# Kernel optimization log

Measured on AMD Instinct MI355X. Metric: run time of the kernel, lower is better.

## Reference

```python
import jax, jax.numpy as jnp
import numpy as np

N = 8192
E = 131072
IN = 512
H = 8
C = 128
HC = H * C
EPS = 1e-5
NEG_SLOPE = 0.2


def _gatv2(x, src, dst, Wl, bl, Wr, br, att, bias):
    """GATv2Conv (PyG semantics, concat=True, self-loops already in src/dst)."""
    n = x.shape[0]
    xl = (x @ Wl + bl).reshape(n, H, C)  # source transform (lin_l)
    xr = (x @ Wr + br).reshape(n, H, C)  # dest transform (lin_r)
    m = xl[src] + xr[dst]                # [E,H,C] per-edge message
    e = jnp.einsum('ehc,hc->eh', jax.nn.leaky_relu(m, NEG_SLOPE), att)  # [E,H]
    # segment softmax over destination nodes
    emax = jax.ops.segment_max(e, dst, num_segments=n)
    w = jnp.exp(e - emax[dst])
    denom = jax.ops.segment_sum(w, dst, num_segments=n)
    alpha = w / denom[dst]               # [E,H]
    out = jax.ops.segment_sum(alpha[:, :, None] * xl[src], dst, num_segments=n)
    return out.reshape(n, HC) + bias


def _bn(x, gamma, beta):
    mu = jnp.mean(x, axis=0)
    var = jnp.mean((x - mu) ** 2, axis=0)
    return (x - mu) * jax.lax.rsqrt(var + EPS) * gamma + beta


def setup_inputs() -> dict:
    key = jax.random.key(0)
    ks = jax.random.split(key, 16)
    s = 0.05
    return {
        'x': jax.random.normal(ks[0], (N, IN), jnp.float32),
        'edge_index': jax.random.randint(ks[1], (2, E), 0, N, jnp.int32),
        'W1l': jax.random.normal(ks[2], (IN, HC), jnp.float32) * s,
        'b1l': jnp.zeros((HC,), jnp.float32),
        'W1r': jax.random.normal(ks[3], (IN, HC), jnp.float32) * s,
        'b1r': jnp.zeros((HC,), jnp.float32),
        'att1': jax.random.normal(ks[4], (H, C), jnp.float32) * s,
        'bias1': jnp.zeros((HC,), jnp.float32),
        'g1': jnp.ones((HC,), jnp.float32),
        'beta1': jnp.zeros((HC,), jnp.float32),
        'W2l': jax.random.normal(ks[5], (HC, HC), jnp.float32) * s,
        'b2l': jnp.zeros((HC,), jnp.float32),
        'W2r': jax.random.normal(ks[6], (HC, HC), jnp.float32) * s,
        'b2r': jnp.zeros((HC,), jnp.float32),
        'att2': jax.random.normal(ks[7], (H, C), jnp.float32) * s,
        'bias2': jnp.zeros((HC,), jnp.float32),
        'g2': jnp.ones((HC,), jnp.float32),
        'beta2': jnp.zeros((HC,), jnp.float32),
    }


def reference(x, edge_index, W1l, b1l, W1r, b1r, att1, bias1, g1, beta1,
              W2l, b2l, W2r, b2r, att2, bias2, g2, beta2):
    n = x.shape[0]
    loops = jnp.arange(n, dtype=edge_index.dtype)
    src = jnp.concatenate([edge_index[0], loops])
    dst = jnp.concatenate([edge_index[1], loops])
    h = _gatv2(x, src, dst, W1l, b1l, W1r, b1r, att1, bias1)
    h = jax.nn.elu(_bn(h, g1, beta1))
    h = _gatv2(h, src, dst, W2l, b2l, W2r, b2r, att2, bias2)
    h = jax.nn.elu(_bn(h, g2, beta2))
    return h
```

## Files before the change

kernel.cpp:

```cpp
#include <hip/hip_runtime.h>
#include <stdint.h>

#define NN     8192
#define NEDGE  131072
#define NETOT  (NEDGE + NN)
#define K_IN   512
#define HC_    1024
#define NOUT   2048
#define BNEPS  1e-5f
#define SLOPE  0.2f

typedef __bf16 bf16x8 __attribute__((ext_vector_type(8)));
typedef float  f32x4  __attribute__((ext_vector_type(4)));
typedef float  f32x2  __attribute__((ext_vector_type(2)));

__device__ __forceinline__ float bf2f(unsigned short u) {
  union { uint32_t u; float f; } c; c.u = ((uint32_t)u) << 16; return c.f;
}
__device__ __forceinline__ unsigned short f2bf(float f) {
  union { float f; uint32_t u; } c; c.f = f;
  uint32_t r = c.u + 0x7fffu + ((c.u >> 16) & 1u);
  return (unsigned short)(r >> 16);
}
__device__ __forceinline__ f32x2 upk2(uint32_t u) {
  union { uint32_t u; float f; } a, b;
  a.u = u << 16; b.u = u & 0xffff0000u;
  f32x2 r; r.x = a.f; r.y = b.f; return r;
}

__device__ __forceinline__ void gload16(const void* g, void* l) {
  __builtin_amdgcn_global_load_lds(
      (const __attribute__((address_space(1))) uint32_t*)g,
      (__attribute__((address_space(3))) uint32_t*)l, 16, 0, 0);
}

#define SBAR() do { asm volatile("" ::: "memory"); __builtin_amdgcn_s_barrier(); asm volatile("" ::: "memory"); } while (0)

__global__ __launch_bounds__(256) void k_cvt_bf16(const float* __restrict__ in,
                                                  unsigned short* __restrict__ out, int n4) {
  int i = blockIdx.x * 256 + threadIdx.x;
  if (i >= n4) return;
  float4 v = *(const float4*)&in[(size_t)i * 4];
  ushort4 o;
  o.x = f2bf(v.x); o.y = f2bf(v.y); o.z = f2bf(v.z); o.w = f2bf(v.w);
  *(ushort4*)&out[(size_t)i * 4] = o;
}

__global__ __launch_bounds__(256) void k_transpose2_bf16(const float* __restrict__ Wa,
                                                         const float* __restrict__ Wb,
                                                         unsigned short* __restrict__ Wt,
                                                         int K, int N) {
  __shared__ float tile[32][33];
  const float* W = blockIdx.z ? Wb : Wa;
  unsigned short* dst = Wt + (size_t)blockIdx.z * N * K;
  int n0 = blockIdx.x * 32, k0 = blockIdx.y * 32;
  int tx = threadIdx.x & 31, ty = threadIdx.x >> 5;
  for (int i = ty; i < 32; i += 8)
    tile[i][tx] = W[(size_t)(k0 + i) * N + n0 + tx];
  __syncthreads();
  for (int i = ty; i < 32; i += 8)
    dst[(size_t)(n0 + i) * K + k0 + tx] = f2bf(tile[tx][i]);
}

__global__ __launch_bounds__(256) void k_hist(const int* __restrict__ ei, int* __restrict__ cnt) {
  int i = blockIdx.x * 256 + threadIdx.x;
  if (i >= NETOT) return;
  int d = (i < NEDGE) ? ei[NEDGE + i] : (i - NEDGE);
  atomicAdd(&cnt[d], 1);
}

__global__ __launch_bounds__(256) void k_scan(const int* __restrict__ cnt,
                                              int* __restrict__ rowptr,
                                              int* __restrict__ cursor) {
  __shared__ int part[256];
  int t = threadIdx.x;
  int base = t * 32;
  int s = 0;
  for (int i = 0; i < 32; ++i) s += cnt[base + i];
  part[t] = s;
  __syncthreads();
  for (int off = 1; off < 256; off <<= 1) {
    int u = (t >= off) ? part[t - off] : 0;
    __syncthreads();
    part[t] += u;
    __syncthreads();
  }
  int run = part[t] - s;
  for (int i = 0; i < 32; ++i) {
    rowptr[base + i] = run;
    cursor[base + i] = run;
    run += cnt[base + i];
  }
  if (t == 255) rowptr[NN] = run;
}

__global__ __launch_bounds__(256) void k_scatter(const int* __restrict__ ei,
                                                 int* __restrict__ cursor,
                                                 int* __restrict__ srcs) {
  int i = blockIdx.x * 256 + threadIdx.x;
  if (i >= NETOT) return;
  int s, d;
  if (i < NEDGE) { s = ei[i]; d = ei[NEDGE + i]; }
  else           { s = d = i - NEDGE; }
  int pos = atomicAdd(&cursor[d], 1);
  srcs[pos] = s;
}

__global__ __launch_bounds__(512, 2) void k_gemm256(const unsigned short* __restrict__ A,
                                                    const unsigned short* __restrict__ Bt,
                                                    const float* __restrict__ biasL,
                                                    const float* __restrict__ biasR,
                                                    unsigned short* __restrict__ C,
                                                    int K) {
  __shared__ unsigned short lA[2][256 * 64];
  __shared__ unsigned short lB[2][256 * 64];

  const int bid = blockIdx.x;
  const int xcd = bid & 7, idx = bid >> 3;
  const int m0 = (xcd * 4 + (idx & 3)) * 256;
  const int n0 = (idx >> 2) * 256;

  const int tid = threadIdx.x;
  const int l   = tid & 63;
  const int wv  = tid >> 6;
  const int wm  = wv >> 2, wn = wv & 3;
  const int l15 = l & 15, l4 = l >> 4;

  const int srow = tid >> 3;
  const int ssgk = (tid & 7) ^ (srow & 7);

  const f32x4 vzero = {0.f, 0.f, 0.f, 0.f};
  f32x4 acc[8][4];
#pragma unroll
  for (int i = 0; i < 8; ++i)
#pragma unroll
    for (int j = 0; j < 4; ++j) acc[i][j] = vzero;

  bf16x8 a2[8];
  bf16x8 bb[2][4];

  auto stageA = [&](int kt, int h) {
    const int buf = kt & 1;
    const size_t go = (size_t)(m0 + h * 128 + srow) * K + (size_t)kt * 64 + ssgk * 8;
    unsigned short* lp = &lA[buf][h * 8192 + tid * 8];
    gload16(&A[go], lp);
    gload16(&A[go + (size_t)64 * K], lp + 4096);
  };
  auto stageB = [&](int kt, int h) {
    const int buf = kt & 1;
    const size_t go = (size_t)(n0 + h * 128 + srow) * K + (size_t)kt * 64 + ssgk * 8;
    unsigned short* lp = &lB[buf][h * 8192 + tid * 8];
    gload16(&Bt[go], lp);
    gload16(&Bt[go + (size_t)64 * K], lp + 4096);
  };
  auto readA = [&](int buf, int qm) {
#pragma unroll
    for (int fm = 0; fm < 4; ++fm)
#pragma unroll
      for (int kk = 0; kk < 2; ++kk) {
        int r = wm * 128 + (qm * 4 + fm) * 16 + l15;
        int g = (kk * 4 + l4) ^ (r & 7);
        a2[fm * 2 + kk] = *(const bf16x8*)&lA[buf][r * 64 + g * 8];
      }
  };
  auto readB = [&](int buf, int qn) {
#pragma unroll
    for (int fn = 0; fn < 2; ++fn)
#pragma unroll
      for (int kk = 0; kk < 2; ++kk) {
        int r = wn * 64 + (qn * 2 + fn) * 16 + l15;
        int g = (kk * 4 + l4) ^ (r & 7);
        bb[qn][fn * 2 + kk] = *(const bf16x8*)&lB[buf][r * 64 + g * 8];
      }
  };
  auto quad = [&](int qm, int qn) {
    __builtin_amdgcn_s_setprio(1);
#pragma unroll
    for (int fm = 0; fm < 4; ++fm)
#pragma unroll
      for (int fn = 0; fn < 2; ++fn)
#pragma unroll
        for (int kk = 0; kk < 2; ++kk)
          acc[qm * 4 + fm][qn * 2 + fn] = __builtin_amdgcn_mfma_f32_16x16x32_bf16(
              a2[fm * 2 + kk], bb[qn][fn * 2 + kk], acc[qm * 4 + fm][qn * 2 + fn], 0, 0, 0);
    __builtin_amdgcn_s_setprio(0);
  };

  const int NT = K >> 6;

  stageA(0, 0); stageA(0, 1); stageB(0, 0); stageB(0, 1);
  if (NT > 1) stageA(1, 0);
  asm volatile("s_waitcnt vmcnt(2)" ::: "memory");
  SBAR();

  for (int t = 0; t < NT; ++t) {
    const int buf = t & 1;
    readA(buf, 0); readB(buf, 0);
    if (t + 1 < NT) stageA(t + 1, 1);
    SBAR();
    quad(0, 0);
    SBAR();
    readB(buf, 1);
    if (t + 1 < NT) stageB(t + 1, 0);
    SBAR();
    quad(0, 1);
    SBAR();
    readA(buf, 1);
    if (t + 1 < NT) stageB(t + 1, 1);
    SBAR();
    quad(1, 0);
    SBAR();
    if (t + 2 < NT) stageA(t + 2, 0);
    asm volatile("s_waitcnt vmcnt(2)" ::: "memory");
    SBAR();
    quad(1, 1);
    SBAR();
  }

  const float* bias = (n0 < HC_) ? biasL : (biasR - HC_);
#pragma unroll
  for (int fm = 0; fm < 8; ++fm) {
#pragma unroll
    for (int fn = 0; fn < 4; ++fn) {
      int col = n0 + wn * 64 + fn * 16 + l15;
      float bv = bias[col];
#pragma unroll
      for (int j = 0; j < 4; ++j) {
        int row = m0 + wm * 128 + fm * 16 + l4 * 4 + j;
        C[(size_t)row * NOUT + col] = f2bf(acc[fm][fn][j] + bv);
      }
    }
  }
}

template <bool OUT_BF16>
__global__ __launch_bounds__(256) void k_edge_agg(const unsigned short* __restrict__ XLR,
                                                  const float* __restrict__ att,
                                                  const float* __restrict__ bias,
                                                  const int* __restrict__ rowptr,
                                                  const int* __restrict__ srcs,
                                                  void* __restrict__ outp) {
  const int tid = threadIdx.x;
  const int d   = blockIdx.x * 4 + (tid >> 6);
  const int l   = tid & 63;
  const int c0  = l * 16;

  f32x2 attv[8], xrv[8];
  {
    const f32x2* ap = (const f32x2*)&att[c0];
#pragma unroll
    for (int q = 0; q < 8; ++q) attv[q] = ap[q];
    const uint4* rp = (const uint4*)&XLR[(size_t)d * NOUT + HC_ + c0];
    uint4 u0 = rp[0], u1 = rp[1];
    xrv[0] = upk2(u0.x); xrv[1] = upk2(u0.y); xrv[2] = upk2(u0.z); xrv[3] = upk2(u0.w);
    xrv[4] = upk2(u1.x); xrv[5] = upk2(u1.y); xrv[6] = upk2(u1.z); xrv[7] = upk2(u1.w);
  }

  f32x2 acc[8];
#pragma unroll
  for (int j = 0; j < 8; ++j) acc[j] = (f32x2){0.f, 0.f};
  float den = 0.f;

  const int beg = rowptr[d], end = rowptr[d + 1];

  uint4 A0, A1, B0, B1, C0, C1;
  {
    const uint4* rp = (const uint4*)&XLR[(size_t)srcs[beg] * NOUT + c0];
    A0 = rp[0]; A1 = rp[1];
  }
  if (beg + 1 < end) {
    const uint4* rp = (const uint4*)&XLR[(size_t)srcs[beg + 1] * NOUT + c0];
    B0 = rp[0]; B1 = rp[1];
  }
  if (beg + 2 < end) {
    const uint4* rp = (const uint4*)&XLR[(size_t)srcs[beg + 2] * NOUT + c0];
    C0 = rp[0]; C1 = rp[1];
  }
  int sD = (beg + 3 < end) ? srcs[beg + 3] : 0;
  int sE = (beg + 4 < end) ? srcs[beg + 4] : 0;

  int i = beg;

#define EDGE_STEP(X0, X1)                                                      \
  {                                                                            \
    f32x2 x[8];                                                                \
    x[0] = upk2(X0.x); x[1] = upk2(X0.y); x[2] = upk2(X0.z); x[3] = upk2(X0.w);\
    x[4] = upk2(X1.x); x[5] = upk2(X1.y); x[6] = upk2(X1.z); x[7] = upk2(X1.w);\
    if (i + 3 < end) {                                                         \
      const uint4* rp = (const uint4*)&XLR[(size_t)sD * NOUT + c0];            \
      X0 = rp[0]; X1 = rp[1];                                                  \
    }                                                                          \
    sD = sE;                                                                   \
    if (i + 5 < end) sE = srcs[i + 5];                                         \
    f32x2 ps = (f32x2){0.f, 0.f};                                              \
    _Pragma("unroll")                                                          \
    for (int j = 0; j < 8; ++j) {                                              \
      f32x2 y  = x[j] + xrv[j];                                                \
      f32x2 lr = __builtin_elementwise_max(y, y * SLOPE);                      \
      ps = lr * attv[j] + ps;                                                  \
    }                                                                          \
    float p = ps.x + ps.y;                                                     \
    p += __shfl_xor(p, 1);                                                     \
    p += __shfl_xor(p, 2);                                                     \
    p += __shfl_xor(p, 4);                                                     \
    float wgt = __expf(p);                                                     \
    den += wgt;                                                                \
    f32x2 w2 = (f32x2){wgt, wgt};                                              \
    _Pragma("unroll")                                                          \
    for (int j = 0; j < 8; ++j) acc[j] = w2 * x[j] + acc[j];                   \
    ++i;                                                                       \
  }

  while (true) {
    EDGE_STEP(A0, A1); if (i >= end) break;
    EDGE_STEP(B0, B1); if (i >= end) break;
    EDGE_STEP(C0, C1); if (i >= end) break;
  }
#undef EDGE_STEP

  float inv = 1.0f / den;
  float o[16];
#pragma unroll
  for (int j = 0; j < 8; ++j) {
    f32x2 bv = ((const f32x2*)&bias[c0])[j];
    o[j * 2]     = acc[j].x * inv + bv.x;
    o[j * 2 + 1] = acc[j].y * inv + bv.y;
  }
  if (OUT_BF16) {
    unsigned short* op = (unsigned short*)outp + (size_t)d * HC_ + c0;
    ushort4 u[4];
#pragma unroll
    for (int q = 0; q < 4; ++q) {
      u[q].x = f2bf(o[q * 4 + 0]); u[q].y = f2bf(o[q * 4 + 1]);
      u[q].z = f2bf(o[q * 4 + 2]); u[q].w = f2bf(o[q * 4 + 3]);
      *(ushort4*)&op[q * 4] = u[q];
    }
  } else {
    float* op = (float*)outp + (size_t)d * HC_ + c0;
#pragma unroll
    for (int q = 0; q < 4; ++q) {
      float4 ov = {o[q * 4 + 0], o[q * 4 + 1], o[q * 4 + 2], o[q * 4 + 3]};
      *(float4*)&op[q * 4] = ov;
    }
  }
}

template <bool IN_BF16>
__global__ __launch_bounds__(256) void k_colstats(const void* __restrict__ Xp,
                                                  float* __restrict__ stats) {
  int col = blockIdx.x * 256 + threadIdx.x;
  int r0 = blockIdx.y * 128;
  float s = 0.f, q = 0.f;
  for (int r = r0; r < r0 + 128; ++r) {
    float v = IN_BF16 ? bf2f(((const unsigned short*)Xp)[(size_t)r * HC_ + col])
                      : ((const float*)Xp)[(size_t)r * HC_ + col];
    s += v;
    q += v * v;
  }
  atomicAdd(&stats[col], s);
  atomicAdd(&stats[HC_ + col], q);
}

template <bool IN_BF16, bool OUT_BF16>
__global__ __launch_bounds__(256) void k_bn_elu(const void* __restrict__ Xp,
                                                const float* __restrict__ stats,
                                                const float* __restrict__ gamma,
                                                const float* __restrict__ beta,
                                                void* __restrict__ outp) {
  size_t idx = (size_t)blockIdx.x * 256 + threadIdx.x;
  size_t e0 = idx * 4;
  int col = (int)(e0 & (HC_ - 1));
  float xs[4];
  if (IN_BF16) {
    ushort4 u = *(const ushort4*)&((const unsigned short*)Xp)[e0];
    xs[0] = bf2f(u.x); xs[1] = bf2f(u.y); xs[2] = bf2f(u.z); xs[3] = bf2f(u.w);
  } else {
    float4 xv = *(const float4*)&((const float*)Xp)[e0];
    xs[0] = xv.x; xs[1] = xv.y; xs[2] = xv.z; xs[3] = xv.w;
  }
  float os[4];
  const float rn = 1.0f / (float)NN;
#pragma unroll
  for (int j = 0; j < 4; ++j) {
    int c = col + j;
    float mu = stats[c] * rn;
    float var = stats[HC_ + c] * rn - mu * mu;
    float v = (xs[j] - mu) * rsqrtf(var + BNEPS) * gamma[c] + beta[c];
    os[j] = v > 0.f ? v : (__expf(v) - 1.f);
  }
  if (OUT_BF16) {
    ushort4 o;
    o.x = f2bf(os[0]); o.y = f2bf(os[1]); o.z = f2bf(os[2]); o.w = f2bf(os[3]);
    *(ushort4*)&((unsigned short*)outp)[e0] = o;
  } else {
    float4 o = {os[0], os[1], os[2], os[3]};
    *(float4*)&((float*)outp)[e0] = o;
  }
}

extern "C" void kernel_launch(void* const* d_in, const int* in_sizes, int n_in,
                              void* d_out, int out_size, void* d_ws, size_t ws_size,
                              hipStream_t stream) {
  const float* x     = (const float*)d_in[0];
  const int*   ei    = (const int*)d_in[1];
  const float* W1l   = (const float*)d_in[2];
  const float* b1l   = (const float*)d_in[3];
  const float* W1r   = (const float*)d_in[4];
  const float* b1r   = (const float*)d_in[5];
  const float* att1  = (const float*)d_in[6];
  const float* bias1 = (const float*)d_in[7];
  const float* g1    = (const float*)d_in[8];
  const float* be1   = (const float*)d_in[9];
  const float* W2l   = (const float*)d_in[10];
  const float* b2l   = (const float*)d_in[11];
  const float* W2r   = (const float*)d_in[12];
  const float* b2r   = (const float*)d_in[13];
  const float* att2  = (const float*)d_in[14];
  const float* bias2 = (const float*)d_in[15];
  const float* g2    = (const float*)d_in[16];
  const float* be2   = (const float*)d_in[17];
  float* out = (float*)d_out;

  char* wsb = (char*)d_ws;
  size_t o = 0;
  auto alloc = [&](size_t b) {
    void* p = wsb + o;
    o = (o + b + 255) & ~(size_t)255;
    return p;
  };
  unsigned short* xbf  = (unsigned short*)alloc((size_t)NN * K_IN * 2);
  unsigned short* wT1  = (unsigned short*)alloc((size_t)NOUT * K_IN * 2);
  unsigned short* wT2  = (unsigned short*)alloc((size_t)NOUT * HC_ * 2);
  unsigned short* XLR  = (unsigned short*)alloc((size_t)NN * NOUT * 2);
  unsigned short* h0   = (unsigned short*)alloc((size_t)NN * HC_ * 2);
  int* cnt     = (int*)alloc((size_t)NN * 4);
  int* rowptr  = (int*)alloc((size_t)(NN + 1) * 4);
  int* cursor  = (int*)alloc((size_t)NN * 4);
  int* srcs    = (int*)alloc((size_t)NETOT * 4);
  float* stats = (float*)alloc((size_t)2 * HC_ * 4);

  hipMemsetAsync(cnt, 0, (size_t)NN * 4, stream);
  hipMemsetAsync(stats, 0, (size_t)2 * HC_ * 4, stream);

  k_cvt_bf16<<<(NN * K_IN / 4 + 255) / 256, 256, 0, stream>>>(x, xbf, NN * K_IN / 4);
  k_transpose2_bf16<<<dim3(HC_ / 32, K_IN / 32, 2), 256, 0, stream>>>(W1l, W1r, wT1, K_IN, HC_);
  k_transpose2_bf16<<<dim3(HC_ / 32, HC_ / 32, 2), 256, 0, stream>>>(W2l, W2r, wT2, HC_, HC_);

  k_hist<<<(NETOT + 255) / 256, 256, 0, stream>>>(ei, cnt);
  k_scan<<<1, 256, 0, stream>>>(cnt, rowptr, cursor);
  k_scatter<<<(NETOT + 255) / 256, 256, 0, stream>>>(ei, cursor, srcs);

  k_gemm256<<<256, 512, 0, stream>>>(xbf, wT1, b1l, b1r, XLR, K_IN);
  k_edge_agg<true><<<NN / 4, 256, 0, stream>>>(XLR, att1, bias1, rowptr, srcs, h0);
  k_colstats<true><<<dim3(HC_ / 256, NN / 128), 256, 0, stream>>>(h0, stats);
  k_bn_elu<true, true><<<NN * HC_ / 4 / 256, 256, 0, stream>>>(h0, stats, g1, be1, h0);

  k_gemm256<<<256, 512, 0, stream>>>(h0, wT2, b2l, b2r, XLR, HC_);
  k_edge_agg<true><<<NN / 4, 256, 0, stream>>>(XLR, att2, bias2, rowptr, srcs, h0);
  hipMemsetAsync(stats, 0, (size_t)2 * HC_ * 4, stream);
  k_colstats<true><<<dim3(HC_ / 256, NN / 128), 256, 0, stream>>>(h0, stats);
  k_bn_elu<true, false><<<NN * HC_ / 4 / 256, 256, 0, stream>>>(h0, stats, g2, be2, out);
}
```

Baseline: 248.6 us.

## Split each destination node across two waves in edge aggregation

New measurement: 233.3 us, median of 3. -6.2%, faster.

```diff
diff --git a/kernel.cpp b/kernel.cpp
--- a/kernel.cpp
+++ b/kernel.cpp
@@ -234,114 +234,99 @@
 }
 
 template <bool OUT_BF16>
-__global__ __launch_bounds__(256) void k_edge_agg(const unsigned short* __restrict__ XLR,
-                                                  const float* __restrict__ att,
-                                                  const float* __restrict__ bias,
-                                                  const int* __restrict__ rowptr,
-                                                  const int* __restrict__ srcs,
-                                                  void* __restrict__ outp) {
-  const int tid = threadIdx.x;
-  const int d   = blockIdx.x * 4 + (tid >> 6);
-  const int l   = tid & 63;
-  const int c0  = l * 16;
-
-  f32x2 attv[8], xrv[8];
+__global__ __launch_bounds__(256, 8) void k_edge_agg(const unsigned short* __restrict__ XLR,
+                                                     const float* __restrict__ att,
+                                                     const float* __restrict__ bias,
+                                                     const int* __restrict__ rowptr,
+                                                     const int* __restrict__ srcs,
+                                                     void* __restrict__ outp) {
+  const int tid  = threadIdx.x;
+  const int wv   = tid >> 6;
+  const int d    = blockIdx.x * 2 + (wv >> 1);
+  const int half = wv & 1;
+  const int l    = tid & 63;
+  const int c0   = half * 512 + l * 8;
+
+  f32x2 attv[4], xrv[4];
   {
     const f32x2* ap = (const f32x2*)&att[c0];
-#pragma unroll
-    for (int q = 0; q < 8; ++q) attv[q] = ap[q];
-    const uint4* rp = (const uint4*)&XLR[(size_t)d * NOUT + HC_ + c0];
-    uint4 u0 = rp[0], u1 = rp[1];
-    xrv[0] = upk2(u0.x); xrv[1] = upk2(u0.y); xrv[2] = upk2(u0.z); xrv[3] = upk2(u0.w);
-    xrv[4] = upk2(u1.x); xrv[5] = upk2(u1.y); xrv[6] = upk2(u1.z); xrv[7] = upk2(u1.w);
-  }
-
-  f32x2 acc[8];
-#pragma unroll
-  for (int j = 0; j < 8; ++j) acc[j] = (f32x2){0.f, 0.f};
+    attv[0] = ap[0]; attv[1] = ap[1]; attv[2] = ap[2]; attv[3] = ap[3];
+    uint4 u = *(const uint4*)&XLR[(size_t)d * NOUT + HC_ + c0];
+    xrv[0] = upk2(u.x); xrv[1] = upk2(u.y); xrv[2] = upk2(u.z); xrv[3] = upk2(u.w);
+  }
+
+  f32x2 acc0 = {0.f, 0.f}, acc1 = {0.f, 0.f}, acc2 = {0.f, 0.f}, acc3 = {0.f, 0.f};
   float den = 0.f;
 
-  const int beg = rowptr[d], end = rowptr[d + 1];
-
-  uint4 A0, A1, B0, B1, C0, C1;
-  {
-    const uint4* rp = (const uint4*)&XLR[(size_t)srcs[beg] * NOUT + c0];
-    A0 = rp[0]; A1 = rp[1];
-  }
-  if (beg + 1 < end) {
-    const uint4* rp = (const uint4*)&XLR[(size_t)srcs[beg + 1] * NOUT + c0];
-    B0 = rp[0]; B1 = rp[1];
-  }
-  if (beg + 2 < end) {
-    const uint4* rp = (const uint4*)&XLR[(size_t)srcs[beg + 2] * NOUT + c0];
-    C0 = rp[0]; C1 = rp[1];
-  }
-  int sD = (beg + 3 < end) ? srcs[beg + 3] : 0;
-  int sE = (beg + 4 < end) ? srcs[beg + 4] : 0;
+  const int beg = __builtin_amdgcn_readfirstlane(rowptr[d]);
+  const int end = __builtin_amdgcn_readfirstlane(rowptr[d + 1]);
+  const int e1  = end - 1;
+
+  auto rowp = [&](int s) { return (const uint4*)&XLR[(size_t)s * NOUT + c0]; };
+  auto cl   = [&](int i) { return i < e1 ? i : e1; };
+
+  uint4 R0 = *rowp(srcs[beg]);
+  uint4 R1 = *rowp(srcs[cl(beg + 1)]);
+  uint4 R2 = *rowp(srcs[cl(beg + 2)]);
+  int sN1 = srcs[cl(beg + 3)];
+  int sN2 = srcs[cl(beg + 4)];
 
   int i = beg;
 
-#define EDGE_STEP(X0, X1)                                                      \
+#define STEP(R)                                                                \
   {                                                                            \
-    f32x2 x[8];                                                                \
-    x[0] = upk2(X0.x); x[1] = upk2(X0.y); x[2] = upk2(X0.z); x[3] = upk2(X0.w);\
-    x[4] = upk2(X1.x); x[5] = upk2(X1.y); x[6] = upk2(X1.z); x[7] = upk2(X1.w);\
-    if (i + 3 < end) {                                                         \
-      const uint4* rp = (const uint4*)&XLR[(size_t)sD * NOUT + c0];            \
-      X0 = rp[0]; X1 = rp[1];                                                  \
-    }                                                                          \
-    sD = sE;                                                                   \
-    if (i + 5 < end) sE = srcs[i + 5];                                         \
-    f32x2 ps = (f32x2){0.f, 0.f};                                              \
-    _Pragma("unroll")                                                          \
-    for (int j = 0; j < 8; ++j) {                                              \
-      f32x2 y  = x[j] + xrv[j];                                                \
-      f32x2 lr = __builtin_elementwise_max(y, y * SLOPE);                      \
-      ps = lr * attv[j] + ps;                                                  \
-    }                                                                          \
+    f32x2 x0 = upk2(R.x), x1 = upk2(R.y), x2 = upk2(R.z), x3 = upk2(R.w);      \
+    R = *rowp(sN1);                                                            \
+    sN1 = sN2;                                                                 \
+    sN2 = srcs[cl(i + 5)];                                                     \
+    f32x2 ps = {0.f, 0.f}, y;                                                  \
+    y = x0 + xrv[0]; ps = __builtin_elementwise_max(y, y * SLOPE) * attv[0] + ps; \
+    y = x1 + xrv[1]; ps = __builtin_elementwise_max(y, y * SLOPE) * attv[1] + ps; \
+    y = x2 + xrv[2]; ps = __builtin_elementwise_max(y, y * SLOPE) * attv[2] + ps; \
+    y = x3 + xrv[3]; ps = __builtin_elementwise_max(y, y * SLOPE) * attv[3] + ps; \
     float p = ps.x + ps.y;                                                     \
     p += __shfl_xor(p, 1);                                                     \
     p += __shfl_xor(p, 2);                                                     \
     p += __shfl_xor(p, 4);                                                     \
+    p += __shfl_xor(p, 8);                                                     \
     float wgt = __expf(p);                                                     \
     den += wgt;                                                                \
-    f32x2 w2 = (f32x2){wgt, wgt};                                              \
-    _Pragma("unroll")                                                          \
-    for (int j = 0; j < 8; ++j) acc[j] = w2 * x[j] + acc[j];                   \
+    f32x2 w2 = {wgt, wgt};                                                     \
+    acc0 = w2 * x0 + acc0;                                                     \
+    acc1 = w2 * x1 + acc1;                                                     \
+    acc2 = w2 * x2 + acc2;                                                     \
+    acc3 = w2 * x3 + acc3;                                                     \
     ++i;                                                                       \
   }
 
   while (true) {
-    EDGE_STEP(A0, A1); if (i >= end) break;
-    EDGE_STEP(B0, B1); if (i >= end) break;
-    EDGE_STEP(C0, C1); if (i >= end) break;
-  }
-#undef EDGE_STEP
-
-  float inv = 1.0f / den;
-  float o[16];
-#pragma unroll
-  for (int j = 0; j < 8; ++j) {
-    f32x2 bv = ((const f32x2*)&bias[c0])[j];
-    o[j * 2]     = acc[j].x * inv + bv.x;
-    o[j * 2 + 1] = acc[j].y * inv + bv.y;
-  }
+    STEP(R0); if (i == end) break;
+    STEP(R1); if (i == end) break;
+    STEP(R2); if (i == end) break;
+  }
+#undef STEP
+
+  const float inv = 1.0f / den;
+  const f32x2* bp = (const f32x2*)&bias[c0];
+  float o[8];
+  o[0] = acc0.x * inv + bp[0].x; o[1] = acc0.y * inv + bp[0].y;
+  o[2] = acc1.x * inv + bp[1].x; o[3] = acc1.y * inv + bp[1].y;
+  o[4] = acc2.x * inv + bp[2].x; o[5] = acc2.y * inv + bp[2].y;
+  o[6] = acc3.x * inv + bp[3].x; o[7] = acc3.y * inv + bp[3].y;
+
   if (OUT_BF16) {
     unsigned short* op = (unsigned short*)outp + (size_t)d * HC_ + c0;
-    ushort4 u[4];
-#pragma unroll
-    for (int q = 0; q < 4; ++q) {
-      u[q].x = f2bf(o[q * 4 + 0]); u[q].y = f2bf(o[q * 4 + 1]);
-      u[q].z = f2bf(o[q * 4 + 2]); u[q].w = f2bf(o[q * 4 + 3]);
-      *(ushort4*)&op[q * 4] = u[q];
-    }
+    ushort4 u0, u1;
+    u0.x = f2bf(o[0]); u0.y = f2bf(o[1]); u0.z = f2bf(o[2]); u0.w = f2bf(o[3]);
+    u1.x = f2bf(o[4]); u1.y = f2bf(o[5]); u1.z = f2bf(o[6]); u1.w = f2bf(o[7]);
+    *(ushort4*)&op[0] = u0;
+    *(ushort4*)&op[4] = u1;
   } else {
     float* op = (float*)outp + (size_t)d * HC_ + c0;
-#pragma unroll
-    for (int q = 0; q < 4; ++q) {
-      float4 ov = {o[q * 4 + 0], o[q * 4 + 1], o[q * 4 + 2], o[q * 4 + 3]};
-      *(float4*)&op[q * 4] = ov;
-    }
+    float4 v0 = {o[0], o[1], o[2], o[3]};
+    float4 v1 = {o[4], o[5], o[6], o[7]};
+    *(float4*)&op[0] = v0;
+    *(float4*)&op[4] = v1;
   }
 }
 
@@ -451,12 +436,12 @@
   k_scatter<<<(NETOT + 255) / 256, 256, 0, stream>>>(ei, cursor, srcs);
 
   k_gemm256<<<256, 512, 0, stream>>>(xbf, wT1, b1l, b1r, XLR, K_IN);
-  k_edge_agg<true><<<NN / 4, 256, 0, stream>>>(XLR, att1, bias1, rowptr, srcs, h0);
+  k_edge_agg<true><<<NN / 2, 256, 0, stream>>>(XLR, att1, bias1, rowptr, srcs, h0);
   k_colstats<true><<<dim3(HC_ / 256, NN / 128), 256, 0, stream>>>(h0, stats);
   k_bn_elu<true, true><<<NN * HC_ / 4 / 256, 256, 0, stream>>>(h0, stats, g1, be1, h0);
 
   k_gemm256<<<256, 512, 0, stream>>>(h0, wT2, b2l, b2r, XLR, HC_);
-  k_edge_agg<true><<<NN / 4, 256, 0, stream>>>(XLR, att2, bias2, rowptr, srcs, h0);
+  k_edge_agg<true><<<NN / 2, 256, 0, stream>>>(XLR, att2, bias2, rowptr, srcs, h0);
   hipMemsetAsync(stats, 0, (size_t)2 * HC_ * 4, stream);
   k_colstats<true><<<dim3(HC_ / 256, NN / 128), 256, 0, stream>>>(h0, stats);
   k_bn_elu<true, false><<<NN * HC_ / 4 / 256, 256, 0, stream>>>(h0, stats, g2, be2, out);
```
